# Optimization experiments

Hardware: AMD Instinct MI355X
Metric: run time of the kernel (lower is better)

Reference implementation:

```python
import jax, jax.numpy as jnp
import numpy as np

N_NODES = 50000
N_EDGES = 800000
IN_DIM = 256
HID = [256, 128]
NEG_SLOPE = 0.01  # F.leaky_relu default


def setup_inputs() -> dict:
    key = jax.random.key(0)
    ks = jax.random.split(key, 8)
    x = jax.random.normal(ks[0], (N_NODES, IN_DIM), dtype=jnp.float32)
    w1 = jax.random.normal(ks[1], (IN_DIM, HID[0]), dtype=jnp.float32) * (1.0 / np.sqrt(IN_DIM))
    b1 = jnp.zeros((HID[0],), dtype=jnp.float32)
    w2 = jax.random.normal(ks[2], (HID[0], HID[1]), dtype=jnp.float32) * (1.0 / np.sqrt(HID[0]))
    b2 = jnp.zeros((HID[1],), dtype=jnp.float32)
    src = jax.random.randint(ks[3], (N_EDGES,), 0, N_NODES, dtype=jnp.int32)
    dst = jax.random.randint(ks[4], (N_EDGES,), 0, N_NODES, dtype=jnp.int32)
    edge_weight = jax.random.uniform(ks[5], (N_EDGES,), dtype=jnp.float32)
    return {"x": x, "w1": w1, "b1": b1, "w2": w2, "b2": b2,
            "src": src, "dst": dst, "edge_weight": edge_weight}


def _gcn_layer(h, w, b, src, dst, ew, n_nodes):
    # GraphConvolution: support = h @ W ; out = spmm(adj, support) + b
    support = h @ w                              # [N, d_out]
    msg = support[src] * ew[:, None]             # [E, d_out] gather + scale
    agg = jax.ops.segment_sum(msg, dst, num_segments=n_nodes)  # [N, d_out]
    return agg + b


def reference(x, w1, b1, w2, b2, src, dst, edge_weight):
    # layer 1: GCN -> leaky_relu -> dropout(eval: identity)
    h = _gcn_layer(x, w1, b1, src, dst, edge_weight, N_NODES)
    h = jax.nn.leaky_relu(h, NEG_SLOPE)
    # layer 2
    h = _gcn_layer(h, w2, b2, src, dst, edge_weight, N_NODES)
    h = jax.nn.leaky_relu(h, NEG_SLOPE)
    return h
```

## Files before the change

### kernel.cpp

```cpp
#include <hip/hip_runtime.h>

#define NEG_SLOPE 0.01f

constexpr int N_NODES_C = 50000;
constexpr int N_EDGES_C = 800000;
constexpr int M_PAD = 50048;
constexpr int META_CAP = 950016;

typedef short bf16x8 __attribute__((ext_vector_type(8)));
typedef float f32x4 __attribute__((ext_vector_type(4)));

__device__ inline unsigned short f2bf(float f) {
  unsigned int u = __float_as_uint(f);
  u += 0x7FFF + ((u >> 16) & 1);
  return (unsigned short)(u >> 16);
}
__device__ inline float bf2f(unsigned int h16) {
  return __uint_as_float(h16 << 16);
}

constexpr int NB_CONV4 = (N_NODES_C * 64) / 1024;
constexpr int NB_Z = 1;
constexpr int NB_W1 = (256 * 256) / 256;
constexpr int NB_W2 = (256 * 128) / 256;
constexpr int NB_HIST = ((N_EDGES_C / 4) + 255) / 256;
constexpr int NB_NONH = NB_CONV4 + NB_Z + NB_W1 + NB_W2;
constexpr int NB_PRE = NB_NONH + NB_HIST;
constexpr int HIST_REGION = NB_HIST * 4;

__global__ __launch_bounds__(256) void pre_kernel(
    const float* __restrict__ x, const float* __restrict__ w1,
    const float* __restrict__ w2, const int* __restrict__ dst,
    unsigned short* __restrict__ xb, unsigned short* __restrict__ w1T,
    unsigned short* __restrict__ w2T, int* __restrict__ counts) {
  const int bx = blockIdx.x;
  const int tid = threadIdx.x;
  int l, isHist = 0, h = 0;
  if (bx < HIST_REGION) {
    if ((bx & 3) == 3) { isHist = 1; h = bx >> 2; l = 0; }
    else l = bx - ((bx + 1) >> 2);
  } else {
    l = bx - NB_HIST;
  }

  if (isHist) {
    int e = (h * 256 + tid) * 4;
    if (e < N_EDGES_C) {
      int4 d4 = *(const int4*)(dst + e);
      atomicAdd(&counts[d4.x], 1);
      atomicAdd(&counts[d4.y], 1);
      atomicAdd(&counts[d4.z], 1);
      atomicAdd(&counts[d4.w], 1);
    }
  } else if (l < NB_CONV4) {
    const float4* xv = (const float4*)x;
#pragma unroll
    for (int i = 0; i < 4; ++i) {
      int g = l * 1024 + i * 256 + tid;
      float4 f = xv[g];
      uint2 o;
      o.x = f2bf(f.x) | ((unsigned)f2bf(f.y) << 16);
      o.y = f2bf(f.z) | ((unsigned)f2bf(f.w) << 16);
      *(uint2*)(xb + (size_t)g * 4) = o;
    }
  } else if (l == NB_CONV4) {
    unsigned short* base = xb + (size_t)N_NODES_C * 256;
    uint4 z = make_uint4(0, 0, 0, 0);
#pragma unroll
    for (int i = 0; i < 6; ++i)
      *(uint4*)(base + (size_t)(i * 256 + tid) * 8) = z;
  } else if (l < NB_CONV4 + NB_Z + NB_W1) {
    int idx = (l - NB_CONV4 - NB_Z) * 256 + tid;
    int n = idx >> 8, k = idx & 255;
    w1T[idx] = f2bf(w1[(size_t)k * 256 + n]);
  } else {
    int idx = (l - NB_CONV4 - NB_Z - NB_W1) * 256 + tid;
    int n = idx >> 8, k = idx & 255;
    w2T[idx] = f2bf(w2[(size_t)k * 128 + n]);
  }
}

constexpr int NB_NODE = (N_NODES_C + 255) / 256;
constexpr int NB_SCAT = (M_PAD + 255) / 256;

__global__ __launch_bounds__(256) void hist_kernel(const int* __restrict__ counts,
                                                   int* __restrict__ hist2,
                                                   int* __restrict__ ehist,
                                                   int* __restrict__ blk_cnt,
                                                   int* __restrict__ blk_e63) {
  __shared__ int lh[64], le[64];
  const int t = threadIdx.x;
  if (t < 64) { lh[t] = 0; le[t] = 0; }
  __syncthreads();
  const int i = blockIdx.x * 256 + t;
  if (i < N_NODES_C) {
    int d = counts[i];
    int bin = d < 63 ? d : 63;
    atomicAdd(&lh[bin], 1);
    atomicAdd(&le[bin], (d + 3) & ~3);
  }
  __syncthreads();
  if (t < 64) {
    if (lh[t]) atomicAdd(&hist2[t], lh[t]);
    if (le[t]) atomicAdd(&ehist[t], le[t]);
    blk_cnt[blockIdx.x * 64 + t] = lh[t];
    if (t == 63) blk_e63[blockIdx.x] = le[63];
  }
}

__global__ __launch_bounds__(256) void scatter_kernel(
    const int* __restrict__ counts, const int* __restrict__ hist2,
    const int* __restrict__ ehist, const int* __restrict__ blk_cnt,
    const int* __restrict__ blk_e63, int* __restrict__ perm,
    int* __restrict__ nstart, int* __restrict__ ndeg,
    int* __restrict__ cursor, unsigned* __restrict__ s_meta) {
  __shared__ int nbase[64], ebase[64], boffn[64], wcnt[4][64], we63s[4];
  __shared__ int boffe63;
  const int t = threadIdx.x;
  const int wv = t >> 6, lane = t & 63;

  if (t < 64) {
    int hv = hist2[t], ev = ehist[t];
    int xs = hv, xe = ev;
#pragma unroll
    for (int off = 1; off < 64; off <<= 1) {
      int a = __shfl_up(xs, off);
      int b = __shfl_up(xe, off);
      if (lane >= off) { xs += a; xe += b; }
    }
    nbase[t] = xs - hv;
    ebase[t] = xe - ev;
    int bn = 0;
    for (int b = 0; b < (int)blockIdx.x; ++b) bn += blk_cnt[b * 64 + t];
    boffn[t] = bn;
  }
  if (t == 64) {
    int be = 0;
    for (int b = 0; b < (int)blockIdx.x; ++b) be += blk_e63[b];
    boffe63 = be;
  }

  const int idx = blockIdx.x * 256 + t;
  int d = -1, bin = 0, d4 = 0;
  if (idx < N_NODES_C) {
    d = counts[idx];
    bin = d < 63 ? d : 63;
    d4 = (d + 3) & ~3;
  } else if (idx < M_PAD) {
    perm[idx] = idx;
    nstart[idx] = 0;
    ndeg[idx] = 0;
  }

  int rank_w = 0, mycnt = 0;
  for (int B = 0; B < 64; ++B) {
    unsigned long long m = __ballot(d >= 0 && bin == B);
    if (d >= 0 && bin == B)
      rank_w = __popcll(m & ((1ull << lane) - 1));
    if (lane == B) mycnt = __popcll(m);
  }
  int c63 = (d >= 0 && bin == 63) ? d4 : 0;
  int sc = c63;
#pragma unroll
  for (int off = 1; off < 64; off <<= 1) {
    int u = __shfl_up(sc, off);
    if (lane >= off) sc += u;
  }
  const int excl63 = sc - c63;
  const int tot63 = __shfl(sc, 63);
  wcnt[wv][lane] = mycnt;
  if (lane == 0) we63s[wv] = tot63;
  __syncthreads();

  if (d >= 0) {
    int rank_blk = rank_w;
    int e63off = excl63;
    for (int w = 0; w < wv; ++w) {
      rank_blk += wcnt[w][bin];
      e63off += we63s[w];
    }
    const int grank = nbase[bin] + boffn[bin] + rank_blk;
    const int d4b = (bin + 3) & ~3;
    const int estart = (bin < 63)
        ? ebase[bin] + (boffn[bin] + rank_blk) * d4b
        : ebase[63] + boffe63 + e63off;
    perm[grank] = idx;
    nstart[grank] = estart;
    ndeg[grank] = d;
    cursor[idx] = estart;
    for (int j = d; j < d4; ++j) s_meta[estart + j] = 0;
  }
}


#define GLOAD_LDS16(g, l)                                              \
  __builtin_amdgcn_global_load_lds(                                    \
      (__attribute__((address_space(1))) void*)(g),                    \
      (__attribute__((address_space(3))) void*)(l), 16, 0, 0)

__device__ __forceinline__ void gemm_tile(
    const unsigned short* __restrict__ A,
    const unsigned short* __restrict__ BT,
    unsigned short* __restrict__ C,
    int N, int ldc, int row0, int col0, short* Asm, short* Bsm) {
  constexpr int K = 256;
  const int tid = threadIdx.x;
  const int lane = tid & 63, wave = tid >> 6;
  const int wm = wave & 1, wn = wave >> 1;

  const int ch0 = wave * 2, ch1 = wave * 2 + 1;
  const int o0 = ch0 * 512 + lane * 8;
  const int o1 = ch1 * 512 + lane * 8;
  const int r0 = o0 >> 5, c0 = o0 & 31;
  const int r1 = o1 >> 5, c1 = o1 & 31;

  f32x4 acc[4][4] = {};

  for (int k0 = 0; k0 < K; k0 += 32) {
    GLOAD_LDS16(A + (size_t)(row0 + r0) * K + k0 + c0, &Asm[ch0 * 512]);
    GLOAD_LDS16(A + (size_t)(row0 + r1) * K + k0 + c1, &Asm[ch1 * 512]);
    GLOAD_LDS16(BT + (size_t)(col0 + r0) * K + k0 + c0, &Bsm[ch0 * 512]);
    GLOAD_LDS16(BT + (size_t)(col0 + r1) * K + k0 + c1, &Bsm[ch1 * 512]);
    __builtin_amdgcn_s_waitcnt(0);
    __syncthreads();

    bf16x8 af[4], bf[4];
#pragma unroll
    for (int mt = 0; mt < 4; ++mt)
      af[mt] = *(const bf16x8*)&Asm[(wm * 64 + mt * 16 + (lane & 15)) * 32 + (lane >> 4) * 8];
#pragma unroll
    for (int nt = 0; nt < 4; ++nt)
      bf[nt] = *(const bf16x8*)&Bsm[(wn * 64 + nt * 16 + (lane & 15)) * 32 + (lane >> 4) * 8];
#pragma unroll
    for (int mt = 0; mt < 4; ++mt)
#pragma unroll
      for (int nt = 0; nt < 4; ++nt)
        acc[mt][nt] = __builtin_amdgcn_mfma_f32_16x16x32_bf16(af[mt], bf[nt], acc[mt][nt], 0, 0, 0);
    __syncthreads();
  }

  const int cl = lane & 15, rq = (lane >> 4) * 4;
#pragma unroll
  for (int mt = 0; mt < 4; ++mt) {
    const int rbase = row0 + wm * 64 + mt * 16 + rq;
#pragma unroll
    for (int nt = 0; nt < 4; ++nt) {
      const int col = col0 + wn * 64 + nt * 16 + cl;
#pragma unroll
      for (int i = 0; i < 4; ++i)
        C[(size_t)(rbase + i) * ldc + col] = f2bf(acc[mt][nt][i]);
    }
  }
}

constexpr int NB_GEMM1 = 2 * (M_PAD / 128);
constexpr int NB_FILL = ((N_EDGES_C / 4) + 255) / 256;

__global__ __launch_bounds__(256) void fill_gemm1_kernel(
    const unsigned short* __restrict__ A, const unsigned short* __restrict__ BT,
    unsigned short* __restrict__ C, const int* __restrict__ src,
    const int* __restrict__ dst, const float* __restrict__ ew,
    int* __restrict__ cursor, unsigned* __restrict__ s_meta) {
  __shared__ short Asm[128 * 32];
  __shared__ short Bsm[128 * 32];
  const int b = blockIdx.x;
  if ((b & 1) == 0) {
    const int t = b >> 1;
    gemm_tile(A, BT, C, 256, 256, (t >> 1) * 128, (t & 1) * 128, Asm, Bsm);
  } else {
    const int g = (b >> 1) * 256 + threadIdx.x;
    const int e = g * 4;
    if (e < N_EDGES_C) {
      int4 d4 = *(const int4*)(dst + e);
      int4 s4 = *(const int4*)(src + e);
      float4 w4 = *(const float4*)(ew + e);
      unsigned m0 = (unsigned)s4.x | ((unsigned)f2bf(w4.x) << 16);
      unsigned m1 = (unsigned)s4.y | ((unsigned)f2bf(w4.y) << 16);
      unsigned m2 = (unsigned)s4.z | ((unsigned)f2bf(w4.z) << 16);
      unsigned m3 = (unsigned)s4.w | ((unsigned)f2bf(w4.w) << 16);
      int p0 = atomicAdd(&cursor[d4.x], 1);
      int p1 = atomicAdd(&cursor[d4.y], 1);
      int p2 = atomicAdd(&cursor[d4.z], 1);
      int p3 = atomicAdd(&cursor[d4.w], 1);
      s_meta[p0] = m0;
      s_meta[p1] = m1;
      s_meta[p2] = m2;
      s_meta[p3] = m3;
    }
  }
}

__global__ __launch_bounds__(256) void gemm2_kernel(
    const unsigned short* __restrict__ A, const unsigned short* __restrict__ BT,
    unsigned short* __restrict__ C) {
  __shared__ short Asm[128 * 32];
  __shared__ short Bsm[128 * 32];
  gemm_tile(A, BT, C, 128, 128, blockIdx.x * 128, 0, Asm, Bsm);
}


__device__ __forceinline__ void rfma_256(float* acc, unsigned m,
                                         const unsigned short* __restrict__ tp) {
  uint2 v = *(const uint2*)(tp + (size_t)(m & 0xffffu) * 256);
  float wt = bf2f(m >> 16);
  acc[0] += bf2f(v.x & 0xffffu) * wt;
  acc[1] += bf2f(v.x >> 16) * wt;
  acc[2] += bf2f(v.y & 0xffffu) * wt;
  acc[3] += bf2f(v.y >> 16) * wt;
}

__device__ __forceinline__ void rfma_128(float* acc, unsigned m,
                                         const unsigned short* __restrict__ tp) {
  unsigned v = *(const unsigned*)(tp + (size_t)(m & 0xffffu) * 128);
  float wt = bf2f(m >> 16);
  acc[0] += bf2f(v & 0xffffu) * wt;
  acc[1] += bf2f(v >> 16) * wt;
}

template <int OUT_D, bool OUT_BF16>
__global__ __launch_bounds__(256) void agg_row_kernel(
    const unsigned short* __restrict__ sup,
    const unsigned* __restrict__ s_meta,
    const int* __restrict__ nstart, const int* __restrict__ ndeg,
    const int* __restrict__ perm, const float* __restrict__ bias,
    unsigned short* __restrict__ out_bf, float* __restrict__ out_f, int n_total) {
  constexpr int DPL = OUT_D / 64;
  const int tid = threadIdx.x;
  const int wv = tid >> 6;
  const int lane = tid & 63;
  const int idx = blockIdx.x * 4 + wv;
  if (idx >= n_total) return;
  const int n = perm[idx];
  const bool valid = n < N_NODES_C;
  const unsigned short* tp = sup + lane * DPL;

  float acc[DPL] = {};
  const int s = nstart[idx];
  const int nq = (ndeg[idx] + 3) >> 2;
  const uint4* mp = (const uint4*)(s_meta + s);

#define RFMA(mm)                              \
  do {                                        \
    if (OUT_D == 256) rfma_256(acc, mm, tp);  \
    else rfma_128(acc, mm, tp);               \
  } while (0)

  if (nq > 0) {
    uint4 m0 = mp[0];
    uint4 m1 = (nq > 1) ? mp[1] : make_uint4(0, 0, 0, 0);
    int q = 0;
    for (; q + 2 < nq; q += 2) {
      uint4 p0 = mp[q + 2];
      uint4 p1 = mp[q + 3];
      RFMA(m0.x); RFMA(m0.y); RFMA(m0.z); RFMA(m0.w);
      RFMA(m1.x); RFMA(m1.y); RFMA(m1.z); RFMA(m1.w);
      m0 = p0;
      m1 = p1;
    }
    RFMA(m0.x); RFMA(m0.y); RFMA(m0.z); RFMA(m0.w);
    if (q + 1 < nq) { RFMA(m1.x); RFMA(m1.y); RFMA(m1.z); RFMA(m1.w); }
  }
#undef RFMA

  const int dbase = lane * DPL;
  if (OUT_BF16) {
    unsigned short o[DPL];
#pragma unroll
    for (int j = 0; j < DPL; ++j) {
      if (valid) {
        float v = acc[j] + bias[dbase + j];
        v = v >= 0.f ? v : NEG_SLOPE * v;
        o[j] = f2bf(v);
      } else {
        o[j] = 0;
      }
    }
    uint2 pk;
    pk.x = o[0] | ((unsigned)o[1] << 16);
    pk.y = o[2] | ((unsigned)o[3] << 16);
    *(uint2*)(out_bf + (size_t)n * OUT_D + dbase) = pk;
  } else if (valid) {
    float r[DPL];
#pragma unroll
    for (int j = 0; j < DPL; ++j) {
      float v = acc[j] + bias[dbase + j];
      r[j] = v >= 0.f ? v : NEG_SLOPE * v;
    }
    *(float2*)(out_f + (size_t)n * OUT_D + dbase) = make_float2(r[0], r[1]);
  }
}


extern "C" void kernel_launch(void* const* d_in, const int* in_sizes, int n_in,
                              void* d_out, int out_size, void* d_ws, size_t ws_size,
                              hipStream_t stream) {
  const float* x  = (const float*)d_in[0];
  const float* w1 = (const float*)d_in[1];
  const float* b1 = (const float*)d_in[2];
  const float* w2 = (const float*)d_in[3];
  const float* b2 = (const float*)d_in[4];
  const int*   src = (const int*)d_in[5];
  const int*   dst = (const int*)d_in[6];
  const float* ew  = (const float*)d_in[7];
  float* out = (float*)d_out;

  unsigned short* xb   = (unsigned short*)d_ws;
  unsigned short* a2b  = xb + (size_t)M_PAD * 256;
  unsigned short* sup1 = a2b + (size_t)M_PAD * 256;
  unsigned short* sup2 = sup1 + (size_t)M_PAD * 256;
  unsigned short* w1T  = sup2 + (size_t)M_PAD * 128;
  unsigned short* w2T  = w1T + 256 * 256;
  int* counts  = (int*)(w2T + 128 * 256);
  int* cursor  = counts + N_NODES_C;
  int* perm    = cursor + N_NODES_C;
  int* nstart  = perm + M_PAD;
  int* ndeg    = nstart + M_PAD;
  int* hist2   = ndeg + M_PAD;
  int* ehist   = hist2 + 64;
  int* zspare  = ehist + 64;
  int* blk_cnt = zspare + 128;
  int* blk_e63 = blk_cnt + NB_NODE * 64;
  unsigned* s_meta = (unsigned*)(blk_e63 + NB_NODE);

  hipMemsetAsync(counts, 0, N_NODES_C * sizeof(int), stream);
  hipMemsetAsync(hist2, 0, 256 * sizeof(int), stream);
  pre_kernel<<<NB_PRE, 256, 0, stream>>>(x, w1, w2, dst, xb, w1T, w2T, counts);

  hist_kernel<<<NB_NODE, 256, 0, stream>>>(counts, hist2, ehist, blk_cnt, blk_e63);
  scatter_kernel<<<NB_SCAT, 256, 0, stream>>>(counts, hist2, ehist, blk_cnt,
                                              blk_e63, perm, nstart, ndeg,
                                              cursor, s_meta);

  fill_gemm1_kernel<<<NB_GEMM1 + NB_FILL, 256, 0, stream>>>(
      xb, w1T, sup1, src, dst, ew, cursor, s_meta);

  agg_row_kernel<256, true><<<M_PAD / 4, 256, 0, stream>>>(
      sup1, s_meta, nstart, ndeg, perm, b1, a2b, nullptr, M_PAD);

  gemm2_kernel<<<M_PAD / 128, 256, 0, stream>>>(a2b, w2T, sup2);
  agg_row_kernel<128, false><<<N_NODES_C / 4, 256, 0, stream>>>(
      sup2, s_meta, nstart, ndeg, perm, b2, nullptr, out, N_NODES_C);
}
```

Baseline: 316.0 us.

## Replace degree-sorted node permutation with plain prefix-scan CSR layout

Drops the degree-bucketed histogram/scatter that sorted nodes by degree into a permutation, and replaces it with a simple two-phase exclusive scan over padded degrees that gives each node its CSR start in natural order. Aggregation now indexes nodes directly and reads degrees from counts, removing the perm and ndeg arrays and one memset. This simplifies preprocessing and removes the serial per-block offset loops, but gives up the degree-sorted ordering that kept waves within a block load-balanced during aggregation.

```diff
diff --git a/kernel.cpp b/kernel.cpp
--- a/kernel.cpp
+++ b/kernel.cpp
@@ -80,115 +80,56 @@
   }
 }
 
-constexpr int NB_NODE = (N_NODES_C + 255) / 256;
-constexpr int NB_SCAT = (M_PAD + 255) / 256;
-
-__global__ __launch_bounds__(256) void hist_kernel(const int* __restrict__ counts,
-                                                   int* __restrict__ hist2,
-                                                   int* __restrict__ ehist,
-                                                   int* __restrict__ blk_cnt,
-                                                   int* __restrict__ blk_e63) {
-  __shared__ int lh[64], le[64];
+constexpr int N_SCAN_BLKS = (N_NODES_C + 255) / 256;
+
+__global__ __launch_bounds__(256) void scan_phase_a(const int* __restrict__ counts,
+                                                    int* __restrict__ partial,
+                                                    int* __restrict__ blk_sums) {
+  __shared__ int s[256];
   const int t = threadIdx.x;
-  if (t < 64) { lh[t] = 0; le[t] = 0; }
+  const int i = blockIdx.x * 256 + t;
+  const int d = (i < N_NODES_C) ? counts[i] : 0;
+  const int p = (d + 3) & ~3;
+  s[t] = p;
+  __syncthreads();
+  for (int off = 1; off < 256; off <<= 1) {
+    int u = (t >= off) ? s[t - off] : 0;
+    __syncthreads();
+    s[t] += u;
+    __syncthreads();
+  }
+  if (i < N_NODES_C) partial[i] = s[t] - p;
+  if (t == 255) blk_sums[blockIdx.x] = s[255];
+}
+
+__global__ __launch_bounds__(256) void scan_phase_bc(const int* __restrict__ counts,
+                                                     const int* __restrict__ partial,
+                                                     const int* __restrict__ blk_sums,
+                                                     int* __restrict__ nstart,
+                                                     int* __restrict__ cursor,
+                                                     unsigned* __restrict__ s_meta) {
+  __shared__ int s[256];
+  __shared__ int blk_excl;
+  const int t = threadIdx.x;
+  const int v = (t < N_SCAN_BLKS) ? blk_sums[t] : 0;
+  s[t] = v;
+  __syncthreads();
+  for (int off = 1; off < 256; off <<= 1) {
+    int u = (t >= off) ? s[t - off] : 0;
+    __syncthreads();
+    s[t] += u;
+    __syncthreads();
+  }
+  if (t == (int)blockIdx.x) blk_excl = s[t] - v;
   __syncthreads();
   const int i = blockIdx.x * 256 + t;
   if (i < N_NODES_C) {
-    int d = counts[i];
-    int bin = d < 63 ? d : 63;
-    atomicAdd(&lh[bin], 1);
-    atomicAdd(&le[bin], (d + 3) & ~3);
-  }
-  __syncthreads();
-  if (t < 64) {
-    if (lh[t]) atomicAdd(&hist2[t], lh[t]);
-    if (le[t]) atomicAdd(&ehist[t], le[t]);
-    blk_cnt[blockIdx.x * 64 + t] = lh[t];
-    if (t == 63) blk_e63[blockIdx.x] = le[63];
-  }
-}
-
-__global__ __launch_bounds__(256) void scatter_kernel(
-    const int* __restrict__ counts, const int* __restrict__ hist2,
-    const int* __restrict__ ehist, const int* __restrict__ blk_cnt,
-    const int* __restrict__ blk_e63, int* __restrict__ perm,
-    int* __restrict__ nstart, int* __restrict__ ndeg,
-    int* __restrict__ cursor, unsigned* __restrict__ s_meta) {
-  __shared__ int nbase[64], ebase[64], boffn[64], wcnt[4][64], we63s[4];
-  __shared__ int boffe63;
-  const int t = threadIdx.x;
-  const int wv = t >> 6, lane = t & 63;
-
-  if (t < 64) {
-    int hv = hist2[t], ev = ehist[t];
-    int xs = hv, xe = ev;
-#pragma unroll
-    for (int off = 1; off < 64; off <<= 1) {
-      int a = __shfl_up(xs, off);
-      int b = __shfl_up(xe, off);
-      if (lane >= off) { xs += a; xe += b; }
-    }
-    nbase[t] = xs - hv;
-    ebase[t] = xe - ev;
-    int bn = 0;
-    for (int b = 0; b < (int)blockIdx.x; ++b) bn += blk_cnt[b * 64 + t];
-    boffn[t] = bn;
-  }
-  if (t == 64) {
-    int be = 0;
-    for (int b = 0; b < (int)blockIdx.x; ++b) be += blk_e63[b];
-    boffe63 = be;
-  }
-
-  const int idx = blockIdx.x * 256 + t;
-  int d = -1, bin = 0, d4 = 0;
-  if (idx < N_NODES_C) {
-    d = counts[idx];
-    bin = d < 63 ? d : 63;
-    d4 = (d + 3) & ~3;
-  } else if (idx < M_PAD) {
-    perm[idx] = idx;
-    nstart[idx] = 0;
-    ndeg[idx] = 0;
-  }
-
-  int rank_w = 0, mycnt = 0;
-  for (int B = 0; B < 64; ++B) {
-    unsigned long long m = __ballot(d >= 0 && bin == B);
-    if (d >= 0 && bin == B)
-      rank_w = __popcll(m & ((1ull << lane) - 1));
-    if (lane == B) mycnt = __popcll(m);
-  }
-  int c63 = (d >= 0 && bin == 63) ? d4 : 0;
-  int sc = c63;
-#pragma unroll
-  for (int off = 1; off < 64; off <<= 1) {
-    int u = __shfl_up(sc, off);
-    if (lane >= off) sc += u;
-  }
-  const int excl63 = sc - c63;
-  const int tot63 = __shfl(sc, 63);
-  wcnt[wv][lane] = mycnt;
-  if (lane == 0) we63s[wv] = tot63;
-  __syncthreads();
-
-  if (d >= 0) {
-    int rank_blk = rank_w;
-    int e63off = excl63;
-    for (int w = 0; w < wv; ++w) {
-      rank_blk += wcnt[w][bin];
-      e63off += we63s[w];
-    }
-    const int grank = nbase[bin] + boffn[bin] + rank_blk;
-    const int d4b = (bin + 3) & ~3;
-    const int estart = (bin < 63)
-        ? ebase[bin] + (boffn[bin] + rank_blk) * d4b
-        : ebase[63] + boffe63 + e63off;
-    perm[grank] = idx;
-    nstart[grank] = estart;
-    ndeg[grank] = d;
-    cursor[idx] = estart;
-    for (int j = d; j < d4; ++j) s_meta[estart + j] = 0;
+    const int d = counts[i];
+    const int d4 = (d + 3) & ~3;
+    const int start = partial[i] + blk_excl;
+    nstart[i] = start;
+    cursor[i] = start;
+    for (int j = d; j < d4; ++j) s_meta[start + j] = 0;
   }
 }
 
@@ -321,22 +262,25 @@
 __global__ __launch_bounds__(256) void agg_row_kernel(
     const unsigned short* __restrict__ sup,
     const unsigned* __restrict__ s_meta,
-    const int* __restrict__ nstart, const int* __restrict__ ndeg,
-    const int* __restrict__ perm, const float* __restrict__ bias,
+    const int* __restrict__ nstart, const int* __restrict__ counts,
+    const float* __restrict__ bias,
     unsigned short* __restrict__ out_bf, float* __restrict__ out_f, int n_total) {
   constexpr int DPL = OUT_D / 64;
   const int tid = threadIdx.x;
   const int wv = tid >> 6;
   const int lane = tid & 63;
-  const int idx = blockIdx.x * 4 + wv;
-  if (idx >= n_total) return;
-  const int n = perm[idx];
+  const int n = blockIdx.x * 4 + wv;
+  if (n >= n_total) return;
   const bool valid = n < N_NODES_C;
   const unsigned short* tp = sup + lane * DPL;
 
   float acc[DPL] = {};
-  const int s = nstart[idx];
-  const int nq = (ndeg[idx] + 3) >> 2;
+  int s = 0, dg = 0;
+  if (valid) {
+    s = nstart[n];
+    dg = counts[n];
+  }
+  const int nq = (dg + 3) >> 2;
   const uint4* mp = (const uint4*)(s_meta + s);
 
 #define RFMA(mm)                              \
@@ -412,32 +356,25 @@
   unsigned short* w2T  = w1T + 256 * 256;
   int* counts  = (int*)(w2T + 128 * 256);
   int* cursor  = counts + N_NODES_C;
-  int* perm    = cursor + N_NODES_C;
-  int* nstart  = perm + M_PAD;
-  int* ndeg    = nstart + M_PAD;
-  int* hist2   = ndeg + M_PAD;
-  int* ehist   = hist2 + 64;
-  int* zspare  = ehist + 64;
-  int* blk_cnt = zspare + 128;
-  int* blk_e63 = blk_cnt + NB_NODE * 64;
-  unsigned* s_meta = (unsigned*)(blk_e63 + NB_NODE);
+  int* nstart  = cursor + N_NODES_C;
+  int* partial = nstart + N_NODES_C;
+  int* blk_sums= partial + N_NODES_C;
+  unsigned* s_meta = (unsigned*)(blk_sums + 256);
 
   hipMemsetAsync(counts, 0, N_NODES_C * sizeof(int), stream);
-  hipMemsetAsync(hist2, 0, 256 * sizeof(int), stream);
   pre_kernel<<<NB_PRE, 256, 0, stream>>>(x, w1, w2, dst, xb, w1T, w2T, counts);
 
-  hist_kernel<<<NB_NODE, 256, 0, stream>>>(counts, hist2, ehist, blk_cnt, blk_e63);
-  scatter_kernel<<<NB_SCAT, 256, 0, stream>>>(counts, hist2, ehist, blk_cnt,
-                                              blk_e63, perm, nstart, ndeg,
-                                              cursor, s_meta);
+  scan_phase_a<<<N_SCAN_BLKS, 256, 0, stream>>>(counts, partial, blk_sums);
+  scan_phase_bc<<<N_SCAN_BLKS, 256, 0, stream>>>(counts, partial, blk_sums,
+                                                 nstart, cursor, s_meta);
 
   fill_gemm1_kernel<<<NB_GEMM1 + NB_FILL, 256, 0, stream>>>(
       xb, w1T, sup1, src, dst, ew, cursor, s_meta);
 
   agg_row_kernel<256, true><<<M_PAD / 4, 256, 0, stream>>>(
-      sup1, s_meta, nstart, ndeg, perm, b1, a2b, nullptr, M_PAD);
+      sup1, s_meta, nstart, counts, b1, a2b, nullptr, M_PAD);
 
   gemm2_kernel<<<M_PAD / 128, 256, 0, stream>>>(a2b, w2T, sup2);
   agg_row_kernel<128, false><<<N_NODES_C / 4, 256, 0, stream>>>(
-      sup2, s_meta, nstart, ndeg, perm, b2, nullptr, out, N_NODES_C);
-}
+      sup2, s_meta, nstart, counts, b2, nullptr, out, N_NODES_C);
+}
```

Result: faster. 284.1 us (-10.1%).
